# Kernel optimization log

Measured on AMD Instinct MI355X. Metric: run time of the kernel, lower is better.

The kernel has to match this reference:

```python
import jax, jax.numpy as jnp
import numpy as np

N, IN_C, D, H, M = 32768, 256, 64, 4, 4
P, S = 64, 512  # partitions x partition_size, P*S == N
SCALE = float(np.sqrt(D))


def setup_inputs() -> dict:
    key = jax.random.key(0)
    ks = jax.random.split(key, 12)
    lim_q = 1.0 / np.sqrt(IN_C)
    inp = {
        "x": jax.random.normal(ks[0], (N, IN_C), dtype=jnp.float32),
        "partition_indices": jnp.arange(N, dtype=jnp.int32).reshape(P, S),
        "boundary_scores": jax.random.uniform(ks[1], (N,), dtype=jnp.float32),
        "Wq_w": jax.random.uniform(ks[2], (H * D, IN_C), jnp.float32, -lim_q, lim_q),
        "Wq_b": jax.random.uniform(ks[3], (H * D,), jnp.float32, -lim_q, lim_q),
        "Wk_w": jax.random.uniform(ks[4], (H * D, IN_C), jnp.float32, -lim_q, lim_q),
        "Wk_b": jax.random.uniform(ks[5], (H * D,), jnp.float32, -lim_q, lim_q),
        "Wv_w": jax.random.uniform(ks[6], (H * D, IN_C), jnp.float32, -lim_q, lim_q),
        "Wv_b": jax.random.uniform(ks[7], (H * D,), jnp.float32, -lim_q, lim_q),
        "pool_seeds": jax.random.normal(ks[8], (M, H, D), dtype=jnp.float32) * 0.02,
        "alpha_logit": jnp.float32(0.0),
        "boundary_weight": jnp.float32(-1.0),
        "beta_logit": jnp.float32(0.0),
    }
    return inp


def reference(x, partition_indices, boundary_scores, Wq_w, Wq_b, Wk_w, Wk_b,
              Wv_w, Wv_b, pool_seeds, alpha_logit, boundary_weight, beta_logit):
    Q = (x @ Wq_w.T + Wq_b).reshape(N, H, D)
    K = (x @ Wk_w.T + Wk_b).reshape(N, H, D)
    V = (x @ Wv_w.T + Wv_b).reshape(N, H, D)

    # Gather per partition: [P, S, H, D]
    Qp = Q[partition_indices]
    Kp = K[partition_indices]
    Vp = V[partition_indices]

    # Local attention within each partition
    attn_local = jax.nn.softmax(
        jnp.einsum('pshd,pthd->phst', Qp, Kp) / SCALE, axis=-1)
    out_p = jnp.einsum('phst,pthd->pshd', attn_local, Vp)
    out_local = jnp.zeros((N, H, D), dtype=x.dtype).at[partition_indices.reshape(-1)].set(
        out_p.reshape(N, H, D))

    # Seed pooling per partition -> multi-resolution representatives
    pool_attn = jax.nn.softmax(
        jnp.einsum('mhd,pshd->pmhs', pool_seeds, Kp) / SCALE, axis=-1)
    reps_k = jnp.einsum('pmhs,pshd->pmhd', pool_attn, Kp).reshape(P * M, H, D)
    reps_v = jnp.einsum('pmhs,pshd->pmhd', pool_attn, Vp).reshape(P * M, H, D)

    x_local = out_local.mean(axis=1)

    # Global cross-attention over all representatives
    cross_attn = jax.nn.softmax(
        jnp.einsum('nhd,rhd->nhr', Q, reps_k) / SCALE, axis=-1)
    out_global = jnp.einsum('nhr,rhd->nhd', cross_attn, reps_v)
    x_global = out_global.mean(axis=1)

    x_self = V.mean(axis=1)

    alpha = jax.nn.sigmoid(alpha_logit + boundary_weight * boundary_scores)[:, None]
    beta = jax.nn.sigmoid(beta_logit) * 2.0
    return alpha * x_local + (1.0 - alpha) * x_global + beta * x_self
```

## Files before the change

### kernel.cpp

```cpp
#include <hip/hip_runtime.h>
#include <hip/hip_bf16.h>

#define N_TOK 32768
#define INC   256
#define HDIM  256
#define NH    4
#define DH    64
#define NP    64
#define SP    512
#define NM    4
#define NREPS 256
#define INV_SCALE 0.125f

typedef __attribute__((ext_vector_type(8))) __bf16 bf16x8;
typedef __attribute__((ext_vector_type(4))) float  f32x4;

static __device__ __forceinline__ ushort f2bf(float f) {
    __hip_bfloat16 h = __float2bfloat16(f);
    return *reinterpret_cast<ushort*>(&h);
}
static __device__ __forceinline__ float bf2f(ushort u) {
    return __uint_as_float(((uint)u) << 16);
}

#define GL_LDS16(g, l) __builtin_amdgcn_global_load_lds( \
    (const __attribute__((address_space(1))) unsigned int*)(g), \
    (__attribute__((address_space(3))) unsigned int*)(l), 16, 0, 0)

__global__ __launch_bounds__(256, 2) void qkv_mfma(
    const float* __restrict__ x,
    const float* __restrict__ Wq, const float* __restrict__ Wk,
    const float* __restrict__ Wv,
    const float* __restrict__ bq, const float* __restrict__ bk,
    const float* __restrict__ bv,
    ushort* __restrict__ Qb, ushort* __restrict__ Kb, ushort* __restrict__ Vb)
{
    const int bx = blockIdx.x;
    const int by = blockIdx.y;
    const int mat = by >> 1, nh = by & 1;
    const float* Wsel = (mat == 0) ? Wq : (mat == 1) ? Wk : Wv;
    const float* W = Wsel + (size_t)nh * 128 * 256;
    const float* bias = ((mat == 0) ? bq : (mat == 1) ? bk : bv) + nh * 128;
    ushort* outp = (mat == 0) ? Qb : (mat == 1) ? Kb : Vb;
    const float qscale = (mat == 0) ? INV_SCALE : 1.0f;
    const int rowBase = bx * 128;
    const int colBase = nh * 128;

    __shared__ ushort As[128 * 64];
    __shared__ ushort Bs[128 * 64];
    __shared__ ushort Cs[4][32][136];

    const int tid = threadIdx.x, wave = tid >> 6, lane = tid & 63;
    const int ln = lane & 15, lg = lane >> 4;

    f32x4 acc[2][8];
    #pragma unroll
    for (int mt = 0; mt < 2; ++mt)
        #pragma unroll
        for (int nt = 0; nt < 8; ++nt) acc[mt][nt] = (f32x4){0.f, 0.f, 0.f, 0.f};

    for (int k0 = 0; k0 < 256; k0 += 64) {
        __syncthreads();
        #pragma unroll
        for (int i = 0; i < 4; ++i) {
            int f = tid + 256 * i;
            int row = f >> 3, dc = f & 7;
            int pos = (dc ^ (row & 7)) << 3;
            {
                const float* src = &x[(size_t)(rowBase + row) * 256 + k0 + dc * 8];
                float4 a = *(const float4*)&src[0];
                float4 b = *(const float4*)&src[4];
                ushort u[8] = {f2bf(a.x), f2bf(a.y), f2bf(a.z), f2bf(a.w),
                               f2bf(b.x), f2bf(b.y), f2bf(b.z), f2bf(b.w)};
                *(int4*)&As[row * 64 + pos] = *(int4*)u;
            }
            {
                const float* src = &W[(size_t)row * 256 + k0 + dc * 8];
                float4 a = *(const float4*)&src[0];
                float4 b = *(const float4*)&src[4];
                ushort u[8] = {f2bf(a.x), f2bf(a.y), f2bf(a.z), f2bf(a.w),
                               f2bf(b.x), f2bf(b.y), f2bf(b.z), f2bf(b.w)};
                *(int4*)&Bs[row * 64 + pos] = *(int4*)u;
            }
        }
        __syncthreads();

        bf16x8 af[2][2], bfr[8][2];
        #pragma unroll
        for (int mt = 0; mt < 2; ++mt)
            #pragma unroll
            for (int kk = 0; kk < 2; ++kk) {
                int row = wave * 32 + mt * 16 + ln;
                int ch  = (kk * 4 + lg) ^ (row & 7);
                af[mt][kk] = *(const bf16x8*)&As[row * 64 + ch * 8];
            }
        #pragma unroll
        for (int nt = 0; nt < 8; ++nt)
            #pragma unroll
            for (int kk = 0; kk < 2; ++kk) {
                int n  = nt * 16 + ln;
                int ch = (kk * 4 + lg) ^ (n & 7);
                bfr[nt][kk] = *(const bf16x8*)&Bs[n * 64 + ch * 8];
            }
        #pragma unroll
        for (int mt = 0; mt < 2; ++mt)
            #pragma unroll
            for (int nt = 0; nt < 8; ++nt)
                #pragma unroll
                for (int kk = 0; kk < 2; ++kk)
                    acc[mt][nt] = __builtin_amdgcn_mfma_f32_16x16x32_bf16(
                        af[mt][kk], bfr[nt][kk], acc[mt][nt], 0, 0, 0);
    }

    float bvv[8];
    #pragma unroll
    for (int nt = 0; nt < 8; ++nt) bvv[nt] = bias[nt * 16 + ln];
    #pragma unroll
    for (int mt = 0; mt < 2; ++mt)
        #pragma unroll
        for (int nt = 0; nt < 8; ++nt)
            #pragma unroll
            for (int r = 0; r < 4; ++r)
                Cs[wave][mt * 16 + lg * 4 + r][nt * 16 + ln] =
                    f2bf((acc[mt][nt][r] + bvv[nt]) * qscale);
    __syncthreads();
    #pragma unroll
    for (int i = 0; i < 8; ++i) {
        int c = i * 64 + lane;
        int row = c >> 4, ch = c & 15;
        int4 v = *(const int4*)&Cs[wave][row][ch * 8];
        int outRow = rowBase + wave * 32 + row;
        *(int4*)&outp[(size_t)outRow * 256 + colBase + ch * 8] = v;
    }
}

__global__ __launch_bounds__(256) void xself_gemm(
    const float* __restrict__ x, const float* __restrict__ Wv,
    const float* __restrict__ bv, const float* __restrict__ beta_logit,
    float* __restrict__ dout)
{
    __shared__ float xs[64][68];
    __shared__ float wsh[64][68];
    const int rowBase = blockIdx.x * 64;
    const int tid = threadIdx.x;
    const int r = tid >> 4, c = tid & 15;

    float acc[4][4];
    #pragma unroll
    for (int a = 0; a < 4; ++a)
        #pragma unroll
        for (int b = 0; b < 4; ++b) acc[a][b] = 0.f;

    for (int k0 = 0; k0 < 256; k0 += 64) {
        __syncthreads();
        #pragma unroll
        for (int i = 0; i < 4; ++i) {
            int f = tid + 256 * i;
            int m = f >> 4, k4 = (f & 15) * 4;
            *(float4*)&xs[m][k4] = *(const float4*)&x[(size_t)(rowBase + m) * 256 + k0 + k4];
        }
        #pragma unroll
        for (int i = 0; i < 4; ++i) {
            int f = tid + 256 * i;
            int n = f >> 4, k4 = (f & 15) * 4;
            float4 w0 = *(const float4*)&Wv[(size_t)n * 256 + k0 + k4];
            float4 w1 = *(const float4*)&Wv[(size_t)(n + 64) * 256 + k0 + k4];
            float4 w2 = *(const float4*)&Wv[(size_t)(n + 128) * 256 + k0 + k4];
            float4 w3 = *(const float4*)&Wv[(size_t)(n + 192) * 256 + k0 + k4];
            float4 wa;
            wa.x = 0.25f * (w0.x + w1.x + w2.x + w3.x);
            wa.y = 0.25f * (w0.y + w1.y + w2.y + w3.y);
            wa.z = 0.25f * (w0.z + w1.z + w2.z + w3.z);
            wa.w = 0.25f * (w0.w + w1.w + w2.w + w3.w);
            *(float4*)&wsh[n][k4] = wa;
        }
        __syncthreads();
        #pragma unroll
        for (int kk = 0; kk < 64; kk += 2) {
            float2 a2[4], b2[4];
            #pragma unroll
            for (int a = 0; a < 4; ++a) a2[a] = *(const float2*)&xs[r + 16 * a][kk];
            #pragma unroll
            for (int b = 0; b < 4; ++b) b2[b] = *(const float2*)&wsh[c + 16 * b][kk];
            #pragma unroll
            for (int a = 0; a < 4; ++a)
                #pragma unroll
                for (int b = 0; b < 4; ++b)
                    acc[a][b] += a2[a].x * b2[b].x + a2[a].y * b2[b].y;
        }
    }

    const float beta = 2.f / (1.f + __expf(-beta_logit[0]));
    #pragma unroll
    for (int b = 0; b < 4; ++b) {
        int col = c + 16 * b;
        float bavg = 0.25f * (bv[col] + bv[col + 64] + bv[col + 128] + bv[col + 192]);
        #pragma unroll
        for (int a = 0; a < 4; ++a)
            dout[(size_t)(rowBase + r + 16 * a) * 64 + col] = beta * (acc[a][b] + bavg);
    }
}

__global__ __launch_bounds__(512) void pool_reps(
    const ushort* __restrict__ Kb, const ushort* __restrict__ Vb,
    const int* __restrict__ idx, const float* __restrict__ seeds,
    ushort* __restrict__ reps_k, ushort* __restrict__ reps_v)
{
    const int p = ((blockIdx.x & 7) << 3) | (blockIdx.x >> 3);
    const int h = blockIdx.y;
    const int tid = threadIdx.x;
    __shared__ float pexp[NM][SP];
    __shared__ float sums[NM];
    __shared__ float sred[NM][8];
    __shared__ float sd[NM][DH];
    __shared__ int   sidx[SP];

    if (tid < NM * DH) {
        int m = tid >> 6, d = tid & 63;
        sd[m][d] = seeds[(size_t)(m * NH + h) * DH + d];
    }
    sidx[tid] = idx[p * SP + tid];
    __syncthreads();

    const int n_s = sidx[tid];
    float kr[64];
    #pragma unroll
    for (int c = 0; c < 8; ++c) {
        int4 raw = *(const int4*)&Kb[(size_t)n_s * HDIM + h * DH + c * 8];
        const ushort* u = (const ushort*)&raw;
        #pragma unroll
        for (int j = 0; j < 8; ++j) kr[c * 8 + j] = bf2f(u[j]);
    }

    float e[NM];
    #pragma unroll
    for (int m = 0; m < NM; ++m) {
        float s = 0.f;
        #pragma unroll
        for (int d = 0; d < 64; ++d) s += kr[d] * sd[m][d];
        e[m] = __expf(s * INV_SCALE);
        pexp[m][tid] = e[m];
    }
    const int lane = tid & 63, w = tid >> 6;
    #pragma unroll
    for (int m = 0; m < NM; ++m) {
        float v = e[m];
        #pragma unroll
        for (int off = 32; off >= 1; off >>= 1) v += __shfl_xor(v, off);
        if (lane == 0) sred[m][w] = v;
    }
    __syncthreads();
    if (tid < NM) {
        float s = 0.f;
        #pragma unroll
        for (int i = 0; i < 8; ++i) s += sred[tid][i];
        sums[tid] = s;
    }
    __syncthreads();

    const int m = w >> 1, kv = w & 1, d = lane;
    const ushort* src = kv ? Vb : Kb;
    float acc = 0.f;
    #pragma unroll 8
    for (int s = 0; s < SP; ++s)
        acc += pexp[m][s] * bf2f(src[(size_t)sidx[s] * HDIM + h * DH + d]);
    ushort* dst = kv ? reps_v : reps_k;
    dst[(size_t)(p * NM + m) * HDIM + h * DH + d] = f2bf(acc / sums[m]);
}

template<int GATHER>
static __device__ __forceinline__ void attn_pass(
    const ushort* __restrict__ Kp, const ushort* __restrict__ Vp,
    const int* __restrict__ gidx, int nkeys, int hofs,
    ushort* Ks, ushort* Vt, ushort* Pw,
    const bf16x8 (&qf)[2][2], f32x4 (&oa)[4][2], float (&ssum)[2],
    int tid, int wave, int lane, int ln, int lg)
{
    for (int kt0 = 0; kt0 < nkeys; kt0 += 64) {
        __syncthreads();
        #pragma unroll
        for (int i = 0; i < 2; ++i) {
            int r0  = wave * 16 + i * 8;
            int key = r0 + (lane >> 3);
            int dc  = lane & 7;
            int cc  = dc ^ (key & 7);
            int row = GATHER ? gidx[kt0 + key] : (kt0 + key);
            GL_LDS16(&Kp[(size_t)row * HDIM + hofs + cc * 8], &Ks[r0 * 64]);
        }
        {
            int kp = tid & 31, dc = tid >> 5;
            int r0 = GATHER ? gidx[kt0 + 2 * kp]     : (kt0 + 2 * kp);
            int r1 = GATHER ? gidx[kt0 + 2 * kp + 1] : (kt0 + 2 * kp + 1);
            int4 v0 = *(const int4*)&Vp[(size_t)r0 * HDIM + hofs + dc * 8];
            int4 v1 = *(const int4*)&Vp[(size_t)r1 * HDIM + hofs + dc * 8];
            const ushort* u0 = (const ushort*)&v0;
            const ushort* u1 = (const ushort*)&v1;
            #pragma unroll
            for (int j = 0; j < 8; ++j) {
                int d = dc * 8 + j;
                uint pk = (uint)u0[j] | ((uint)u1[j] << 16);
                *(uint*)&Vt[d * 64 + (((kp >> 2) ^ (d & 7)) << 3) + (kp & 3) * 2] = pk;
            }
        }
        __syncthreads();

        #pragma unroll
        for (int ktile = 0; ktile < 4; ++ktile) {
            int kr = ktile * 16 + ln;
            bf16x8 ka0 = *(const bf16x8*)&Ks[kr * 64 + ((lg       ^ (kr & 7)) << 3)];
            bf16x8 ka1 = *(const bf16x8*)&Ks[kr * 64 + (((4 + lg) ^ (kr & 7)) << 3)];
            #pragma unroll
            for (int qt = 0; qt < 2; ++qt) {
                f32x4 s = (f32x4){0.f, 0.f, 0.f, 0.f};
                s = __builtin_amdgcn_mfma_f32_16x16x32_bf16(ka0, qf[qt][0], s, 0, 0, 0);
                s = __builtin_amdgcn_mfma_f32_16x16x32_bf16(ka1, qf[qt][1], s, 0, 0, 0);
                float p0 = __expf(s[0]);
                float p1 = __expf(s[1]);
                float p2 = __expf(s[2]);
                float p3 = __expf(s[3]);
                ssum[qt] += (p0 + p1) + (p2 + p3);
                uint lo = (uint)f2bf(p0) | ((uint)f2bf(p1) << 16);
                uint hi = (uint)f2bf(p2) | ((uint)f2bf(p3) << 16);
                int q  = qt * 16 + ln;
                int k0 = ktile * 16 + lg * 4;
                uint2 pk; pk.x = lo; pk.y = hi;
                *(uint2*)&Pw[q * 64 + (((k0 >> 3) ^ (q & 7)) << 3) + (k0 & 7)] = pk;
            }
        }

        bf16x8 pf[2][2];
        #pragma unroll
        for (int qt = 0; qt < 2; ++qt) {
            int q = qt * 16 + ln;
            #pragma unroll
            for (int kc = 0; kc < 2; ++kc) {
                int k0 = kc * 32 + lg * 8;
                pf[qt][kc] = *(const bf16x8*)&Pw[q * 64 + (((k0 >> 3) ^ (q & 7)) << 3)];
            }
        }
        #pragma unroll
        for (int dt = 0; dt < 4; ++dt) {
            int d = dt * 16 + ln;
            bf16x8 vf[2];
            #pragma unroll
            for (int kc = 0; kc < 2; ++kc) {
                int k0 = kc * 32 + lg * 8;
                vf[kc] = *(const bf16x8*)&Vt[d * 64 + (((k0 >> 3) ^ (d & 7)) << 3)];
            }
            #pragma unroll
            for (int qt = 0; qt < 2; ++qt)
                #pragma unroll
                for (int kc = 0; kc < 2; ++kc)
                    oa[dt][qt] = __builtin_amdgcn_mfma_f32_16x16x32_bf16(
                        vf[kc], pf[qt][kc], oa[dt][qt], 0, 0, 0);
        }
    }
}

__global__ __launch_bounds__(256, 3) void attn_fused(
    const ushort* __restrict__ Qb, const ushort* __restrict__ Kb,
    const ushort* __restrict__ Vb,
    const ushort* __restrict__ repk, const ushort* __restrict__ repv,
    const int* __restrict__ idx, const float* __restrict__ bscore,
    const float* __restrict__ alpha_logit, const float* __restrict__ bweight,
    float* __restrict__ xc)
{
    const int work = ((blockIdx.x & 7) << 5) | (blockIdx.x >> 3);
    const int p = work >> 2, qc = work & 3;
    const int h = blockIdx.y;
    const int hofs = h * DH;
    const int tid  = threadIdx.x;
    const int wave = tid >> 6;
    const int lane = tid & 63;
    const int ln = lane & 15;
    const int lg = lane >> 4;

    __shared__ ushort Ks[64 * 64];
    __shared__ ushort Vt[64 * 64];
    __shared__ ushort Pb[4][32 * 64];
    ushort* Pw = Pb[wave];

    const int* gidx = idx + p * SP;

    bf16x8 qf[2][2];
    int tok[2];
    #pragma unroll
    for (int qt = 0; qt < 2; ++qt) {
        int qj = wave * 32 + qt * 16 + ln;
        int t  = gidx[qc * 128 + qj];
        tok[qt] = t;
        #pragma unroll
        for (int kc = 0; kc < 2; ++kc)
            qf[qt][kc] = *(const bf16x8*)&Qb[(size_t)t * HDIM + hofs + kc * 32 + lg * 8];
    }

    f32x4 oa_l[4][2], oa_g[4][2];
    float ssl[2] = {0.f, 0.f}, ssg[2] = {0.f, 0.f};
    #pragma unroll
    for (int dt = 0; dt < 4; ++dt)
        #pragma unroll
        for (int qt = 0; qt < 2; ++qt) {
            oa_l[dt][qt] = (f32x4){0.f, 0.f, 0.f, 0.f};
            oa_g[dt][qt] = (f32x4){0.f, 0.f, 0.f, 0.f};
        }

    attn_pass<1>(Kb, Vb, gidx, SP, hofs, Ks, Vt, Pw,
                 qf, oa_l, ssl, tid, wave, lane, ln, lg);
    attn_pass<0>(repk, repv, gidx, NREPS, hofs, Ks, Vt, Pw,
                 qf, oa_g, ssg, tid, wave, lane, ln, lg);

    const float al = alpha_logit[0], bw = bweight[0];
    #pragma unroll
    for (int qt = 0; qt < 2; ++qt) {
        float sl = ssl[qt];
        sl += __shfl_xor(sl, 16);
        sl += __shfl_xor(sl, 32);
        float sg = ssg[qt];
        sg += __shfl_xor(sg, 16);
        sg += __shfl_xor(sg, 32);
        float a = 1.f / (1.f + __expf(-(al + bw * bscore[tok[qt]])));
        float wl = a * 0.25f / sl;
        float wg = (1.f - a) * 0.25f / sg;
        float* dst = &xc[((size_t)h * N_TOK + tok[qt]) * DH];
        #pragma unroll
        for (int dt = 0; dt < 4; ++dt) {
            float4 v;
            v.x = oa_l[dt][qt][0] * wl + oa_g[dt][qt][0] * wg;
            v.y = oa_l[dt][qt][1] * wl + oa_g[dt][qt][1] * wg;
            v.z = oa_l[dt][qt][2] * wl + oa_g[dt][qt][2] * wg;
            v.w = oa_l[dt][qt][3] * wl + oa_g[dt][qt][3] * wg;
            *(float4*)&dst[dt * 16 + lg * 4] = v;
        }
    }
}

__global__ __launch_bounds__(256) void combine(
    const float4* __restrict__ xc, float4* __restrict__ dout)
{
    const size_t PL = (size_t)N_TOK * DH / 4;
    const size_t i = (size_t)blockIdx.x * 256 + threadIdx.x;
    float4 a = xc[i], b = xc[i + PL], c = xc[i + 2 * PL], d = xc[i + 3 * PL];
    float4 o = dout[i];
    o.x += a.x + b.x + c.x + d.x;
    o.y += a.y + b.y + c.y + d.y;
    o.z += a.z + b.z + c.z + d.z;
    o.w += a.w + b.w + c.w + d.w;
    dout[i] = o;
}

extern "C" void kernel_launch(void* const* d_in, const int* in_sizes, int n_in,
                              void* d_out, int out_size, void* d_ws, size_t ws_size,
                              hipStream_t stream)
{
    (void)in_sizes; (void)n_in; (void)ws_size; (void)out_size;
    const float* x      = (const float*)d_in[0];
    const int*   idx    = (const int*)d_in[1];
    const float* bscore = (const float*)d_in[2];
    const float* Wq = (const float*)d_in[3]; const float* bq = (const float*)d_in[4];
    const float* Wk = (const float*)d_in[5]; const float* bk = (const float*)d_in[6];
    const float* Wv = (const float*)d_in[7]; const float* bv = (const float*)d_in[8];
    const float* seeds = (const float*)d_in[9];
    const float* al = (const float*)d_in[10];
    const float* bw = (const float*)d_in[11];
    const float* bl = (const float*)d_in[12];
    float* out = (float*)d_out;

    const size_t NE = (size_t)N_TOK * HDIM;
    ushort* Qb    = (ushort*)d_ws;
    ushort* Kb    = Qb + NE;
    ushort* Vb    = Kb + NE;
    ushort* repkb = Vb + NE;
    ushort* repvb = repkb + (size_t)NREPS * HDIM;
    float*  xc    = (float*)(repvb + (size_t)NREPS * HDIM);

    qkv_mfma  <<<dim3(256, 6), 256, 0, stream>>>(x, Wq, Wk, Wv, bq, bk, bv,
                                                 Qb, Kb, Vb);
    xself_gemm<<<512, 256, 0, stream>>>(x, Wv, bv, bl, out);
    pool_reps <<<dim3(NP, NH), 512, 0, stream>>>(Kb, Vb, idx, seeds, repkb, repvb);
    attn_fused<<<dim3(256, NH), 256, 0, stream>>>(Qb, Kb, Vb, repkb, repvb,
                                                  idx, bscore, al, bw, xc);
    combine   <<<2048, 256, 0, stream>>>((const float4*)xc, (float4*)out);
}
```

Baseline: 242.3 us.

## Double-buffer K/V tiles in attention and fold x_self into attention epilogue

The attention pass now double-buffers K and transposed V tiles in shared memory. It prefetches the next tile's K (async to LDS) and V (to registers) while computing the current one, which halves the barriers per tile. Separately, the x_self fp32 GEMM kernel is removed. The beta-weighted head-mean of V is added in the attention epilogue from the bf16 V buffer, and combine no longer reads out. This removes a kernel launch and a full fp32 GEMM pass, but uses bf16 V for x_self, which lowers precision, and doubles LDS use, which may reduce occupancy.

```diff
diff --git a/kernel.cpp b/kernel.cpp
--- a/kernel.cpp
+++ b/kernel.cpp
@@ -134,73 +134,6 @@
     }
 }
 
-__global__ __launch_bounds__(256) void xself_gemm(
-    const float* __restrict__ x, const float* __restrict__ Wv,
-    const float* __restrict__ bv, const float* __restrict__ beta_logit,
-    float* __restrict__ dout)
-{
-    __shared__ float xs[64][68];
-    __shared__ float wsh[64][68];
-    const int rowBase = blockIdx.x * 64;
-    const int tid = threadIdx.x;
-    const int r = tid >> 4, c = tid & 15;
-
-    float acc[4][4];
-    #pragma unroll
-    for (int a = 0; a < 4; ++a)
-        #pragma unroll
-        for (int b = 0; b < 4; ++b) acc[a][b] = 0.f;
-
-    for (int k0 = 0; k0 < 256; k0 += 64) {
-        __syncthreads();
-        #pragma unroll
-        for (int i = 0; i < 4; ++i) {
-            int f = tid + 256 * i;
-            int m = f >> 4, k4 = (f & 15) * 4;
-            *(float4*)&xs[m][k4] = *(const float4*)&x[(size_t)(rowBase + m) * 256 + k0 + k4];
-        }
-        #pragma unroll
-        for (int i = 0; i < 4; ++i) {
-            int f = tid + 256 * i;
-            int n = f >> 4, k4 = (f & 15) * 4;
-            float4 w0 = *(const float4*)&Wv[(size_t)n * 256 + k0 + k4];
-            float4 w1 = *(const float4*)&Wv[(size_t)(n + 64) * 256 + k0 + k4];
-            float4 w2 = *(const float4*)&Wv[(size_t)(n + 128) * 256 + k0 + k4];
-            float4 w3 = *(const float4*)&Wv[(size_t)(n + 192) * 256 + k0 + k4];
-            float4 wa;
-            wa.x = 0.25f * (w0.x + w1.x + w2.x + w3.x);
-            wa.y = 0.25f * (w0.y + w1.y + w2.y + w3.y);
-            wa.z = 0.25f * (w0.z + w1.z + w2.z + w3.z);
-            wa.w = 0.25f * (w0.w + w1.w + w2.w + w3.w);
-            *(float4*)&wsh[n][k4] = wa;
-        }
-        __syncthreads();
-        #pragma unroll
-        for (int kk = 0; kk < 64; kk += 2) {
-            float2 a2[4], b2[4];
-            #pragma unroll
-            for (int a = 0; a < 4; ++a) a2[a] = *(const float2*)&xs[r + 16 * a][kk];
-            #pragma unroll
-            for (int b = 0; b < 4; ++b) b2[b] = *(const float2*)&wsh[c + 16 * b][kk];
-            #pragma unroll
-            for (int a = 0; a < 4; ++a)
-                #pragma unroll
-                for (int b = 0; b < 4; ++b)
-                    acc[a][b] += a2[a].x * b2[b].x + a2[a].y * b2[b].y;
-        }
-    }
-
-    const float beta = 2.f / (1.f + __expf(-beta_logit[0]));
-    #pragma unroll
-    for (int b = 0; b < 4; ++b) {
-        int col = c + 16 * b;
-        float bavg = 0.25f * (bv[col] + bv[col + 64] + bv[col + 128] + bv[col + 192]);
-        #pragma unroll
-        for (int a = 0; a < 4; ++a)
-            dout[(size_t)(rowBase + r + 16 * a) * 64 + col] = beta * (acc[a][b] + bavg);
-    }
-}
-
 __global__ __launch_bounds__(512) void pool_reps(
     const ushort* __restrict__ Kb, const ushort* __restrict__ Vb,
     const int* __restrict__ idx, const float* __restrict__ seeds,
@@ -272,43 +205,65 @@
 static __device__ __forceinline__ void attn_pass(
     const ushort* __restrict__ Kp, const ushort* __restrict__ Vp,
     const int* __restrict__ gidx, int nkeys, int hofs,
-    ushort* Ks, ushort* Vt, ushort* Pw,
+    ushort* Ks0, ushort* Ks1, ushort* Vt0, ushort* Vt1, ushort* Pw,
     const bf16x8 (&qf)[2][2], f32x4 (&oa)[4][2], float (&ssum)[2],
     int tid, int wave, int lane, int ln, int lg)
 {
-    for (int kt0 = 0; kt0 < nkeys; kt0 += 64) {
-        __syncthreads();
+    const int kp = tid & 31, dc = tid >> 5;
+
+    {
         #pragma unroll
         for (int i = 0; i < 2; ++i) {
             int r0  = wave * 16 + i * 8;
             int key = r0 + (lane >> 3);
-            int dc  = lane & 7;
-            int cc  = dc ^ (key & 7);
-            int row = GATHER ? gidx[kt0 + key] : (kt0 + key);
-            GL_LDS16(&Kp[(size_t)row * HDIM + hofs + cc * 8], &Ks[r0 * 64]);
-        }
-        {
-            int kp = tid & 31, dc = tid >> 5;
-            int r0 = GATHER ? gidx[kt0 + 2 * kp]     : (kt0 + 2 * kp);
+            int cc  = (lane & 7) ^ (key & 7);
+            int row = GATHER ? gidx[key] : key;
+            GL_LDS16(&Kp[(size_t)row * HDIM + hofs + cc * 8], &Ks0[r0 * 64]);
+        }
+        int r0 = GATHER ? gidx[2 * kp] : 2 * kp;
+        int r1 = GATHER ? gidx[2 * kp + 1] : 2 * kp + 1;
+        int4 v0 = *(const int4*)&Vp[(size_t)r0 * HDIM + hofs + dc * 8];
+        int4 v1 = *(const int4*)&Vp[(size_t)r1 * HDIM + hofs + dc * 8];
+        const ushort* u0 = (const ushort*)&v0;
+        const ushort* u1 = (const ushort*)&v1;
+        #pragma unroll
+        for (int j = 0; j < 8; ++j) {
+            int d = dc * 8 + j;
+            uint pk = (uint)u0[j] | ((uint)u1[j] << 16);
+            *(uint*)&Vt0[d * 64 + (((kp >> 2) ^ (d & 7)) << 3) + (kp & 3) * 2] = pk;
+        }
+    }
+    __syncthreads();
+
+    const int nt = nkeys >> 6;
+    for (int t = 0; t < nt; ++t) {
+        ushort* KsC = (t & 1) ? Ks1 : Ks0;
+        ushort* VtC = (t & 1) ? Vt1 : Vt0;
+        ushort* KsN = (t & 1) ? Ks0 : Ks1;
+        ushort* VtN = (t & 1) ? Vt0 : Vt1;
+        const bool pfn = (t + 1 < nt);
+        int4 v0, v1;
+        if (pfn) {
+            int kt0 = (t + 1) << 6;
+            #pragma unroll
+            for (int i = 0; i < 2; ++i) {
+                int r0  = wave * 16 + i * 8;
+                int key = r0 + (lane >> 3);
+                int cc  = (lane & 7) ^ (key & 7);
+                int row = GATHER ? gidx[kt0 + key] : (kt0 + key);
+                GL_LDS16(&Kp[(size_t)row * HDIM + hofs + cc * 8], &KsN[r0 * 64]);
+            }
+            int r0 = GATHER ? gidx[kt0 + 2 * kp] : (kt0 + 2 * kp);
             int r1 = GATHER ? gidx[kt0 + 2 * kp + 1] : (kt0 + 2 * kp + 1);
-            int4 v0 = *(const int4*)&Vp[(size_t)r0 * HDIM + hofs + dc * 8];
-            int4 v1 = *(const int4*)&Vp[(size_t)r1 * HDIM + hofs + dc * 8];
-            const ushort* u0 = (const ushort*)&v0;
-            const ushort* u1 = (const ushort*)&v1;
-            #pragma unroll
-            for (int j = 0; j < 8; ++j) {
-                int d = dc * 8 + j;
-                uint pk = (uint)u0[j] | ((uint)u1[j] << 16);
-                *(uint*)&Vt[d * 64 + (((kp >> 2) ^ (d & 7)) << 3) + (kp & 3) * 2] = pk;
-            }
-        }
-        __syncthreads();
+            v0 = *(const int4*)&Vp[(size_t)r0 * HDIM + hofs + dc * 8];
+            v1 = *(const int4*)&Vp[(size_t)r1 * HDIM + hofs + dc * 8];
+        }
 
         #pragma unroll
         for (int ktile = 0; ktile < 4; ++ktile) {
             int kr = ktile * 16 + ln;
-            bf16x8 ka0 = *(const bf16x8*)&Ks[kr * 64 + ((lg       ^ (kr & 7)) << 3)];
-            bf16x8 ka1 = *(const bf16x8*)&Ks[kr * 64 + (((4 + lg) ^ (kr & 7)) << 3)];
+            bf16x8 ka0 = *(const bf16x8*)&KsC[kr * 64 + ((lg       ^ (kr & 7)) << 3)];
+            bf16x8 ka1 = *(const bf16x8*)&KsC[kr * 64 + (((4 + lg) ^ (kr & 7)) << 3)];
             #pragma unroll
             for (int qt = 0; qt < 2; ++qt) {
                 f32x4 s = (f32x4){0.f, 0.f, 0.f, 0.f};
@@ -345,7 +300,7 @@
             #pragma unroll
             for (int kc = 0; kc < 2; ++kc) {
                 int k0 = kc * 32 + lg * 8;
-                vf[kc] = *(const bf16x8*)&Vt[d * 64 + (((k0 >> 3) ^ (d & 7)) << 3)];
+                vf[kc] = *(const bf16x8*)&VtC[d * 64 + (((k0 >> 3) ^ (d & 7)) << 3)];
             }
             #pragma unroll
             for (int qt = 0; qt < 2; ++qt)
@@ -354,6 +309,18 @@
                     oa[dt][qt] = __builtin_amdgcn_mfma_f32_16x16x32_bf16(
                         vf[kc], pf[qt][kc], oa[dt][qt], 0, 0, 0);
         }
+
+        if (pfn) {
+            const ushort* u0 = (const ushort*)&v0;
+            const ushort* u1 = (const ushort*)&v1;
+            #pragma unroll
+            for (int j = 0; j < 8; ++j) {
+                int d = dc * 8 + j;
+                uint pk = (uint)u0[j] | ((uint)u1[j] << 16);
+                *(uint*)&VtN[d * 64 + (((kp >> 2) ^ (d & 7)) << 3) + (kp & 3) * 2] = pk;
+            }
+        }
+        __syncthreads();
     }
 }
 
@@ -363,6 +330,7 @@
     const ushort* __restrict__ repk, const ushort* __restrict__ repv,
     const int* __restrict__ idx, const float* __restrict__ bscore,
     const float* __restrict__ alpha_logit, const float* __restrict__ bweight,
+    const float* __restrict__ beta_logit,
     float* __restrict__ xc)
 {
     const int work = ((blockIdx.x & 7) << 5) | (blockIdx.x >> 3);
@@ -375,8 +343,8 @@
     const int ln = lane & 15;
     const int lg = lane >> 4;
 
-    __shared__ ushort Ks[64 * 64];
-    __shared__ ushort Vt[64 * 64];
+    __shared__ ushort Ks[2][64 * 64];
+    __shared__ ushort Vt[2][64 * 64];
     __shared__ ushort Pb[4][32 * 64];
     ushort* Pw = Pb[wave];
 
@@ -404,12 +372,13 @@
             oa_g[dt][qt] = (f32x4){0.f, 0.f, 0.f, 0.f};
         }
 
-    attn_pass<1>(Kb, Vb, gidx, SP, hofs, Ks, Vt, Pw,
+    attn_pass<1>(Kb, Vb, gidx, SP, hofs, Ks[0], Ks[1], Vt[0], Vt[1], Pw,
                  qf, oa_l, ssl, tid, wave, lane, ln, lg);
-    attn_pass<0>(repk, repv, gidx, NREPS, hofs, Ks, Vt, Pw,
+    attn_pass<0>(repk, repv, gidx, NREPS, hofs, Ks[0], Ks[1], Vt[0], Vt[1], Pw,
                  qf, oa_g, ssg, tid, wave, lane, ln, lg);
 
     const float al = alpha_logit[0], bw = bweight[0];
+    const float beta25 = 0.25f * 2.f / (1.f + __expf(-beta_logit[0]));
     #pragma unroll
     for (int qt = 0; qt < 2; ++qt) {
         float sl = ssl[qt];
@@ -422,13 +391,15 @@
         float wl = a * 0.25f / sl;
         float wg = (1.f - a) * 0.25f / sg;
         float* dst = &xc[((size_t)h * N_TOK + tok[qt]) * DH];
+        const ushort* vsrc = &Vb[(size_t)tok[qt] * HDIM + hofs];
         #pragma unroll
         for (int dt = 0; dt < 4; ++dt) {
+            uint2 vv = *(const uint2*)&vsrc[dt * 16 + lg * 4];
             float4 v;
-            v.x = oa_l[dt][qt][0] * wl + oa_g[dt][qt][0] * wg;
-            v.y = oa_l[dt][qt][1] * wl + oa_g[dt][qt][1] * wg;
-            v.z = oa_l[dt][qt][2] * wl + oa_g[dt][qt][2] * wg;
-            v.w = oa_l[dt][qt][3] * wl + oa_g[dt][qt][3] * wg;
+            v.x = oa_l[dt][qt][0] * wl + oa_g[dt][qt][0] * wg + beta25 * bf2f((ushort)(vv.x & 0xffff));
+            v.y = oa_l[dt][qt][1] * wl + oa_g[dt][qt][1] * wg + beta25 * bf2f((ushort)(vv.x >> 16));
+            v.z = oa_l[dt][qt][2] * wl + oa_g[dt][qt][2] * wg + beta25 * bf2f((ushort)(vv.y & 0xffff));
+            v.w = oa_l[dt][qt][3] * wl + oa_g[dt][qt][3] * wg + beta25 * bf2f((ushort)(vv.y >> 16));
             *(float4*)&dst[dt * 16 + lg * 4] = v;
         }
     }
@@ -440,11 +411,11 @@
     const size_t PL = (size_t)N_TOK * DH / 4;
     const size_t i = (size_t)blockIdx.x * 256 + threadIdx.x;
     float4 a = xc[i], b = xc[i + PL], c = xc[i + 2 * PL], d = xc[i + 3 * PL];
-    float4 o = dout[i];
-    o.x += a.x + b.x + c.x + d.x;
-    o.y += a.y + b.y + c.y + d.y;
-    o.z += a.z + b.z + c.z + d.z;
-    o.w += a.w + b.w + c.w + d.w;
+    float4 o;
+    o.x = a.x + b.x + c.x + d.x;
+    o.y = a.y + b.y + c.y + d.y;
+    o.z = a.z + b.z + c.z + d.z;
+    o.w = a.w + b.w + c.w + d.w;
     dout[i] = o;
 }
 
@@ -473,11 +444,10 @@
     ushort* repvb = repkb + (size_t)NREPS * HDIM;
     float*  xc    = (float*)(repvb + (size_t)NREPS * HDIM);
 
-    qkv_mfma  <<<dim3(256, 6), 256, 0, stream>>>(x, Wq, Wk, Wv, bq, bk, bv,
-                                                 Qb, Kb, Vb);
-    xself_gemm<<<512, 256, 0, stream>>>(x, Wv, bv, bl, out);
-    pool_reps <<<dim3(NP, NH), 512, 0, stream>>>(Kb, Vb, idx, seeds, repkb, repvb);
+    qkv_mfma <<<dim3(256, 6), 256, 0, stream>>>(x, Wq, Wk, Wv, bq, bk, bv,
+                                                Qb, Kb, Vb);
+    pool_reps<<<dim3(NP, NH), 512, 0, stream>>>(Kb, Vb, idx, seeds, repkb, repvb);
     attn_fused<<<dim3(256, NH), 256, 0, stream>>>(Qb, Kb, Vb, repkb, repvb,
-                                                  idx, bscore, al, bw, xc);
-    combine   <<<2048, 256, 0, stream>>>((const float4*)xc, (float4*)out);
-}
+                                                  idx, bscore, al, bw, bl, xc);
+    combine  <<<2048, 256, 0, stream>>>((const float4*)xc, (float4*)out);
+}
```

Result: faster. 208.8 us (-13.8%).
